# Performance work log

Hardware: AMD Instinct MI355X
Metric: run time of the kernel (lower is better)

The kernel has to match this reference:

```python
import jax, jax.numpy as jnp
import numpy as np

B, N, T = 32, 200, 20000  # batchsize, number of 3x3 node blocks, number of (i,j,k) triplets


def setup_inputs() -> dict:
    key = jax.random.key(0)
    k1, k2 = jax.random.split(key)
    H = jax.random.normal(k1, (B, 3 * N, 3 * N), dtype=jnp.float32)
    triplets = jax.random.randint(k2, (T, 3), 0, N)  # node indices (i, j, k)
    return {"H": H, "triplets": triplets}


def reference(H, triplets):
    Bq, S, _ = H.shape
    Nn = S // 3
    # View H as an (N x N) grid of 3x3 blocks: (B, N, N, 3, 3)
    Hb = H.reshape(Bq, Nn, 3, Nn, 3).transpose(0, 1, 3, 2, 4)
    # J_block @ H @ J_block acts block-wise as diag(1,1,-1) @ blk @ diag(1,1,-1)
    s = jnp.array([1.0, 1.0, -1.0], dtype=H.dtype)
    ss = s[:, None] * s[None, :]  # sign mask (3,3)

    i, j, k = triplets[:, 0], triplets[:, 1], triplets[:, 2]
    H_ij = Hb[:, i, j]  # (B, T, 3, 3)
    H_jk = Hb[:, j, k]
    H_ki = Hb[:, k, i]

    # variant 0 = plain block, variant 1 = J-conjugated block
    Aij = jnp.stack([H_ij, H_ij * ss], axis=2)  # (B, T, 2, 3, 3)
    Ajk = jnp.stack([H_jk, H_jk * ss], axis=2)
    Aki = jnp.stack([H_ki, H_ki * ss], axis=2)

    # chain of tiny 3x3 matmuls over all 2*2*2 = 8 variant combinations
    M1 = jnp.einsum('ztapq,ztbqr->ztabpr', Aij, Ajk)          # (B, T, 2, 2, 3, 3)
    comb = jnp.einsum('ztabpr,ztcrs->ztabcps', M1, Aki)       # (B, T, 2, 2, 2, 3, 3)
    comb = comb.reshape(Bq, -1, 8, 3, 3)                      # matches original stack order

    eye = jnp.eye(3, dtype=H.dtype)
    err = jnp.linalg.norm(comb - eye, axis=(-2, -1))          # Frobenius norm -> (B, T, 8)
    return err
```

## Files before the change

kernel.cpp:

```cpp
#include <hip/hip_runtime.h>

#define BQ 32
#define TT 20000
#define NN 200
#define S3 600
#define JSTRIDE 296
#define R_HALFS ((size_t)NN * NN * 288)

typedef float    f32x4 __attribute__((ext_vector_type(4)));
typedef float    f32x2 __attribute__((ext_vector_type(2)));
typedef _Float16 f16x8 __attribute__((ext_vector_type(8)));
typedef _Float16 f16x4 __attribute__((ext_vector_type(4)));

__global__ __launch_bounds__(512) void repack3_kernel(
    const float* __restrict__ H, _Float16* __restrict__ R)
{
    __shared__ _Float16 lds[100 * JSTRIDE];
    const int i   = blockIdx.x >> 1;
    const int jh  = blockIdx.x & 1;
    const int tid = threadIdx.x;

    for (int e = tid; e < 1800; e += 512) {
        int bq  = e / 225;
        int rem = e - bq * 225;
        int p   = rem / 75;
        int c4  = rem - p * 75;
        const float* base = H + (size_t)(3 * i + p) * S3 + jh * 300 + 4 * c4;
        f32x4 v0 = *reinterpret_cast<const f32x4*>(base + (size_t)(bq * 4 + 0) * (S3 * S3));
        f32x4 v1 = *reinterpret_cast<const f32x4*>(base + (size_t)(bq * 4 + 1) * (S3 * S3));
        f32x4 v2 = *reinterpret_cast<const f32x4*>(base + (size_t)(bq * 4 + 2) * (S3 * S3));
        f32x4 v3 = *reinterpret_cast<const f32x4*>(base + (size_t)(bq * 4 + 3) * (S3 * S3));
#pragma unroll
        for (int x = 0; x < 4; ++x) {
            int cl = 4 * c4 + x;
            int jl = cl / 3, q = cl - 3 * jl;
            f16x4 hv;
            hv[0] = (_Float16)v0[x];
            hv[1] = (_Float16)v1[x];
            hv[2] = (_Float16)v2[x];
            hv[3] = (_Float16)v3[x];
            *reinterpret_cast<f16x4*>(&lds[jl * JSTRIDE + (p * 3 + q) * 32 + bq * 4]) = hv;
        }
    }
    __syncthreads();

    f16x8* dst = reinterpret_cast<f16x8*>(R + ((size_t)i * NN + jh * 100) * 288);
    for (int w = tid; w < 3600; w += 512) {
        int jl  = w / 36;
        int rem = w - jl * 36;
        f16x8 v = *reinterpret_cast<const f16x8*>(&lds[jl * JSTRIDE + rem * 8]);
        dst[(size_t)jl * 36 + rem] = v;
    }
}

__device__ __forceinline__ f32x2 pk_sqrt_clamp(f32x2 x)
{
    f32x2 r;
    r.x = sqrtf(fmaxf(x.x, 0.0f));
    r.y = sqrtf(fmaxf(x.y, 0.0f));
    return r;
}

__device__ __forceinline__ void compute_errs_pk(
    const f32x2 Mij[9], const f32x2 Mjk[9], const f32x2 Mki[9], f32x2 res[8])
{
    f32x2 N1[2][9];
#pragma unroll
    for (int p = 0; p < 3; ++p) {
#pragma unroll
        for (int r = 0; r < 3; ++r) {
            f32x2 c = Mij[p*3+0] * Mjk[0*3+r] + Mij[p*3+1] * Mjk[1*3+r];
            f32x2 d = Mij[p*3+2] * Mjk[2*3+r];
            N1[0][p*3+r] = c + d;
            N1[1][p*3+r] = c - d;
        }
    }
    f32x2 err[2][2];
#pragma unroll
    for (int u = 0; u < 2; ++u) {
        f32x2 T2p[9], T2m[9];
#pragma unroll
        for (int p = 0; p < 3; ++p) {
#pragma unroll
            for (int s = 0; s < 3; ++s) {
                f32x2 c = N1[u][p*3+0] * Mki[0*3+s] + N1[u][p*3+1] * Mki[1*3+s];
                f32x2 d = N1[u][p*3+2] * Mki[2*3+s];
                T2p[p*3+s] = c + d;
                T2m[p*3+s] = c - d;
            }
        }
#pragma unroll
        for (int v = 0; v < 2; ++v) {
            const f32x2* T2 = (v == 0) ? T2p : T2m;
            f32x2 ss = T2[0] * T2[0];
#pragma unroll
            for (int e = 1; e < 9; ++e) ss += T2[e] * T2[e];
            f32x2 diag = T2[0] + T2[4] + (((u ^ v) & 1) ? -T2[8] : T2[8]);
            f32x2 e2 = ss - 2.0f * diag + 3.0f;
            err[u][v] = pk_sqrt_clamp(e2);
        }
    }
#pragma unroll
    for (int m = 0; m < 8; ++m) {
        int a = (m >> 2) & 1, bb = (m >> 1) & 1, c = m & 1;
        res[m] = err[a ^ bb][bb ^ c];
    }
}

__global__ __launch_bounds__(256, 2) void gather4_pk_kernel(
    const _Float16* __restrict__ R, const int* __restrict__ trip,
    float* __restrict__ out)
{
    int g  = blockIdx.x * 256 + threadIdx.x;
    int bg = g & 7;
    int t  = g >> 3;

    int i = trip[3 * t + 0];
    int j = trip[3 * t + 1];
    int k = trip[3 * t + 2];

    const f16x4* __restrict__ Rij = reinterpret_cast<const f16x4*>(R) + (size_t)(i * NN + j) * 72 + bg;
    const f16x4* __restrict__ Rjk = reinterpret_cast<const f16x4*>(R) + (size_t)(j * NN + k) * 72 + bg;
    const f16x4* __restrict__ Rki = reinterpret_cast<const f16x4*>(R) + (size_t)(k * NN + i) * 72 + bg;

    f16x4 Aij[9], Ajk[9], Aki[9];
#pragma unroll
    for (int pq = 0; pq < 9; ++pq) {
        Aij[pq] = Rij[pq * 8];
        Ajk[pq] = Rjk[pq * 8];
        Aki[pq] = Rki[pq * 8];
    }

#pragma unroll
    for (int h = 0; h < 2; ++h) {
        f32x2 Mij[9], Mjk[9], Mki[9];
#pragma unroll
        for (int pq = 0; pq < 9; ++pq) {
            Mij[pq] = f32x2{(float)Aij[pq][2*h], (float)Aij[pq][2*h+1]};
            Mjk[pq] = f32x2{(float)Ajk[pq][2*h], (float)Ajk[pq][2*h+1]};
            Mki[pq] = f32x2{(float)Aki[pq][2*h], (float)Aki[pq][2*h+1]};
        }
        f32x2 r2[8];
        compute_errs_pk(Mij, Mjk, Mki, r2);

#pragma unroll
        for (int u2 = 0; u2 < 2; ++u2) {
            int b = 4 * bg + 2 * h + u2;
            f32x4* o4 = reinterpret_cast<f32x4*>(out + ((size_t)b * TT + t) * 8);
            f32x4 lo, hi;
            lo.x = r2[0][u2]; lo.y = r2[1][u2]; lo.z = r2[2][u2]; lo.w = r2[3][u2];
            hi.x = r2[4][u2]; hi.y = r2[5][u2]; hi.z = r2[6][u2]; hi.w = r2[7][u2];
            __builtin_nontemporal_store(lo, o4);
            __builtin_nontemporal_store(hi, o4 + 1);
        }
    }
}

__device__ __forceinline__ void compute_errs(
    const float Mij[9], const float Mjk[9], const float Mki[9], float res[8])
{
    float N1[2][9];
#pragma unroll
    for (int p = 0; p < 3; ++p) {
#pragma unroll
        for (int r = 0; r < 3; ++r) {
            float c = Mij[p*3+0] * Mjk[0*3+r] + Mij[p*3+1] * Mjk[1*3+r];
            float d = Mij[p*3+2] * Mjk[2*3+r];
            N1[0][p*3+r] = c + d;
            N1[1][p*3+r] = c - d;
        }
    }
    float err[2][2];
#pragma unroll
    for (int u = 0; u < 2; ++u) {
        float T2p[9], T2m[9];
#pragma unroll
        for (int p = 0; p < 3; ++p) {
#pragma unroll
            for (int s = 0; s < 3; ++s) {
                float c = N1[u][p*3+0] * Mki[0*3+s] + N1[u][p*3+1] * Mki[1*3+s];
                float d = N1[u][p*3+2] * Mki[2*3+s];
                T2p[p*3+s] = c + d;
                T2m[p*3+s] = c - d;
            }
        }
#pragma unroll
        for (int v = 0; v < 2; ++v) {
            const float* T2 = (v == 0) ? T2p : T2m;
            float ss = 0.0f;
#pragma unroll
            for (int e = 0; e < 9; ++e) ss += T2[e] * T2[e];
            float diag = T2[0] + T2[4] + (((u ^ v) & 1) ? -T2[8] : T2[8]);
            float e2 = ss - 2.0f * diag + 3.0f;
            err[u][v] = sqrtf(fmaxf(e2, 0.0f));
        }
    }
#pragma unroll
    for (int m = 0; m < 8; ++m) {
        int a = (m >> 2) & 1, bb = (m >> 1) & 1, c = m & 1;
        res[m] = err[a ^ bb][bb ^ c];
    }
}

__global__ __launch_bounds__(256) void jcfg_err_direct(
    const float* __restrict__ H,
    const int*   __restrict__ trip,
    float*       __restrict__ out)
{
    int idx = blockIdx.x * blockDim.x + threadIdx.x;
    if (idx >= BQ * TT) return;
    int b = idx / TT;
    int t = idx - b * TT;

    int i = trip[3 * t + 0];
    int j = trip[3 * t + 1];
    int k = trip[3 * t + 2];

    const float* __restrict__ Hb = H + (size_t)b * (S3 * S3);

    float Mij[9], Mjk[9], Mki[9];
    const int ri = 3 * i, rj = 3 * j, rk = 3 * k;
#pragma unroll
    for (int p = 0; p < 3; ++p) {
        __builtin_memcpy(&Mij[3*p], Hb + (size_t)(ri + p) * S3 + rj, 12);
        __builtin_memcpy(&Mjk[3*p], Hb + (size_t)(rj + p) * S3 + rk, 12);
        __builtin_memcpy(&Mki[3*p], Hb + (size_t)(rk + p) * S3 + ri, 12);
    }

    float res[8];
    compute_errs(Mij, Mjk, Mki, res);

    float* o = out + (size_t)idx * 8;
    *reinterpret_cast<float4*>(o)     = make_float4(res[0], res[1], res[2], res[3]);
    *reinterpret_cast<float4*>(o + 4) = make_float4(res[4], res[5], res[6], res[7]);
}

extern "C" void kernel_launch(void* const* d_in, const int* in_sizes, int n_in,
                              void* d_out, int out_size, void* d_ws, size_t ws_size,
                              hipStream_t stream)
{
    const float* H    = (const float*)d_in[0];
    const int*   trip = (const int*)d_in[1];
    float*       out  = (float*)d_out;

    if (ws_size >= R_HALFS * sizeof(_Float16)) {
        _Float16* R = (_Float16*)d_ws;
        repack3_kernel<<<NN * 2, 512, 0, stream>>>(H, R);
        gather4_pk_kernel<<<(TT * 8) / 256, 256, 0, stream>>>(R, trip, out);
    } else {
        const int total = BQ * TT;
        jcfg_err_direct<<<(total + 255) / 256, 256, 0, stream>>>(H, trip, out);
    }
}
```

Before: 29.26 us.

## Split repacked fp16 block table into per-batch-group slices for gather

New measurement: 30.60 us. 1.05x slower.

```diff
diff --git a/kernel.cpp b/kernel.cpp
--- a/kernel.cpp
+++ b/kernel.cpp
@@ -5,14 +5,15 @@
 #define NN 200
 #define S3 600
 #define JSTRIDE 296
-#define R_HALFS ((size_t)NN * NN * 288)
+#define SLICE_HALFS ((size_t)NN * NN * 36)
+#define R_HALFS (8 * SLICE_HALFS)
 
 typedef float    f32x4 __attribute__((ext_vector_type(4)));
 typedef float    f32x2 __attribute__((ext_vector_type(2)));
 typedef _Float16 f16x8 __attribute__((ext_vector_type(8)));
 typedef _Float16 f16x4 __attribute__((ext_vector_type(4)));
 
-__global__ __launch_bounds__(512) void repack3_kernel(
+__global__ __launch_bounds__(512) void repack_sliced_kernel(
     const float* __restrict__ H, _Float16* __restrict__ R)
 {
     __shared__ _Float16 lds[100 * JSTRIDE];
@@ -44,12 +45,21 @@
     }
     __syncthreads();
 
-    f16x8* dst = reinterpret_cast<f16x8*>(R + ((size_t)i * NN + jh * 100) * 288);
-    for (int w = tid; w < 3600; w += 512) {
-        int jl  = w / 36;
-        int rem = w - jl * 36;
-        f16x8 v = *reinterpret_cast<const f16x8*>(&lds[jl * JSTRIDE + rem * 8]);
-        dst[(size_t)jl * 36 + rem] = v;
+    for (int w2 = tid; w2 < 3600; w2 += 512) {
+        int x  = w2 / 450;
+        int w  = w2 - x * 450;
+        int u0 = 2 * w;
+        int u1 = u0 + 1;
+        int jl0 = u0 / 9, pq0 = u0 - jl0 * 9;
+        int jl1 = u1 / 9, pq1 = u1 - jl1 * 9;
+        f16x4 a = *reinterpret_cast<const f16x4*>(&lds[jl0 * JSTRIDE + pq0 * 32 + x * 4]);
+        f16x4 b = *reinterpret_cast<const f16x4*>(&lds[jl1 * JSTRIDE + pq1 * 32 + x * 4]);
+        f16x8 v;
+#pragma unroll
+        for (int z = 0; z < 4; ++z) { v[z] = a[z]; v[z + 4] = b[z]; }
+        f16x8* dst = reinterpret_cast<f16x8*>(
+            R + (size_t)x * SLICE_HALFS + ((size_t)i * NN + jh * 100) * 36);
+        dst[w] = v;
     }
 }
 
@@ -107,28 +117,30 @@
     }
 }
 
-__global__ __launch_bounds__(256, 2) void gather4_pk_kernel(
+__global__ __launch_bounds__(256, 2) void gather_slice_kernel(
     const _Float16* __restrict__ R, const int* __restrict__ trip,
     float* __restrict__ out)
 {
-    int g  = blockIdx.x * 256 + threadIdx.x;
-    int bg = g & 7;
-    int t  = g >> 3;
-
-    int i = trip[3 * t + 0];
-    int j = trip[3 * t + 1];
-    int k = trip[3 * t + 2];
-
-    const f16x4* __restrict__ Rij = reinterpret_cast<const f16x4*>(R) + (size_t)(i * NN + j) * 72 + bg;
-    const f16x4* __restrict__ Rjk = reinterpret_cast<const f16x4*>(R) + (size_t)(j * NN + k) * 72 + bg;
-    const f16x4* __restrict__ Rki = reinterpret_cast<const f16x4*>(R) + (size_t)(k * NN + i) * 72 + bg;
+    const int x   = blockIdx.x & 7;
+    const int seq = blockIdx.x >> 3;
+    const int t   = seq * 256 + threadIdx.x;
+    if (t >= TT) return;
+
+    const int i = trip[3 * t + 0];
+    const int j = trip[3 * t + 1];
+    const int k = trip[3 * t + 2];
+
+    const f16x4* __restrict__ S = reinterpret_cast<const f16x4*>(R + (size_t)x * SLICE_HALFS);
+    const f16x4* __restrict__ Pij = S + (size_t)(i * NN + j) * 9;
+    const f16x4* __restrict__ Pjk = S + (size_t)(j * NN + k) * 9;
+    const f16x4* __restrict__ Pki = S + (size_t)(k * NN + i) * 9;
 
     f16x4 Aij[9], Ajk[9], Aki[9];
 #pragma unroll
     for (int pq = 0; pq < 9; ++pq) {
-        Aij[pq] = Rij[pq * 8];
-        Ajk[pq] = Rjk[pq * 8];
-        Aki[pq] = Rki[pq * 8];
+        Aij[pq] = Pij[pq];
+        Ajk[pq] = Pjk[pq];
+        Aki[pq] = Pki[pq];
     }
 
 #pragma unroll
@@ -145,7 +157,7 @@
 
 #pragma unroll
         for (int u2 = 0; u2 < 2; ++u2) {
-            int b = 4 * bg + 2 * h + u2;
+            int b = 4 * x + 2 * h + u2;
             f32x4* o4 = reinterpret_cast<f32x4*>(out + ((size_t)b * TT + t) * 8);
             f32x4 lo, hi;
             lo.x = r2[0][u2]; lo.y = r2[1][u2]; lo.z = r2[2][u2]; lo.w = r2[3][u2];
@@ -245,8 +257,9 @@
 
     if (ws_size >= R_HALFS * sizeof(_Float16)) {
         _Float16* R = (_Float16*)d_ws;
-        repack3_kernel<<<NN * 2, 512, 0, stream>>>(H, R);
-        gather4_pk_kernel<<<(TT * 8) / 256, 256, 0, stream>>>(R, trip, out);
+        repack_sliced_kernel<<<NN * 2, 512, 0, stream>>>(H, R);
+        const int blocks = 8 * ((TT + 255) / 256);
+        gather_slice_kernel<<<blocks, 256, 0, stream>>>(R, trip, out);
     } else {
         const int total = BQ * TT;
         jcfg_err_direct<<<(total + 255) / 256, 256, 0, stream>>>(H, trip, out);
```
